# Optimization experiments

Measured on AMD Instinct MI355X. Metric: run time of the kernel, lower is better.

Reference implementation:

```python
import jax, jax.numpy as jnp
import numpy as np

EPS = 1e-5
SLOPE = 0.01  # torch LeakyReLU default negative_slope


def _stage(h, W):
    # h: [B, N, k, Cin]; W: [Cout, Cin] (1x1 conv, no bias)
    h = jnp.einsum('bnkc,oc->bnko', h, W)
    # InstanceNorm2d (affine=False): normalize per (batch, channel) over spatial (N, k)
    mean = jnp.mean(h, axis=(1, 2), keepdims=True)
    var = jnp.var(h, axis=(1, 2), keepdims=True)
    h = (h - mean) * jax.lax.rsqrt(var + EPS)
    return jnp.where(h >= 0, h, SLOPE * h)


def setup_inputs() -> dict:
    key = jax.random.key(0)
    k1, k2, k3, k4, k5 = jax.random.split(key, 5)
    B, N, D, K, C = 8, 4096, 64, 20, 64
    x = jax.random.normal(k1, (B, N, D), dtype=jnp.float32)
    ind = jax.random.randint(k2, (B, N, K), 0, B * N, dtype=jnp.int64)
    W1 = jax.random.normal(k3, (C, 2 * D), dtype=jnp.float32) * 0.05
    W2 = jax.random.normal(k4, (C, C), dtype=jnp.float32) * 0.05
    W3 = jax.random.normal(k5, (C, C), dtype=jnp.float32) * 0.05
    return {"x": x, "ind": ind, "W1": W1, "W2": W2, "W3": W3}


def reference(x, ind, W1, W2, W3):
    B, N, D = x.shape
    k = ind.shape[2]
    # Gather neighbors via global (B*N) indices, as in the torch code
    y = x.reshape(B * N, D)[ind.reshape(B * N, k)].reshape(B, N, k, D)  # [B,N,k,D]
    xe = jnp.broadcast_to(x[:, :, None, :], (B, N, k, D))
    feat = jnp.concatenate([y - xe, xe], axis=3)  # [B,N,k,2D]
    h = _stage(feat, W1)
    h = _stage(h, W2)
    h = _stage(h, W3)
    # max-pool over k neighbors -> [B, N, Cout]
    return jnp.max(h, axis=2)
```

## Files before the change

### kernel.cpp

```cpp
#include <hip/hip_runtime.h>

#define BDIM 8
#define NPTS 4096
#define KNEI 20
#define BN (BDIM*NPTS)
#define NKCNT (NPTS*KNEI)
#define EPSI 1e-5f
#define SLOPE 0.01f

typedef __attribute__((ext_vector_type(8))) short bf16x8;
typedef __attribute__((ext_vector_type(4))) float f32x4;
typedef __attribute__((ext_vector_type(4))) unsigned int u32x4;

__device__ __forceinline__ unsigned short f2bf(float f) {
    unsigned u = __builtin_bit_cast(unsigned, f);
    u += 0x7FFFu + ((u >> 16) & 1u);
    return (unsigned short)(u >> 16);
}
__device__ __forceinline__ float bf2f(unsigned short h) {
    unsigned u = ((unsigned)h) << 16;
    return __builtin_bit_cast(float, u);
}

__device__ __forceinline__ void async16(const void* g, void* l) {
    __builtin_amdgcn_global_load_lds(
        (const __attribute__((address_space(1))) unsigned int*)g,
        (__attribute__((address_space(3))) unsigned int*)l, 16, 0, 0);
}

__global__ __launch_bounds__(256) void k0_uv(const float* __restrict__ x,
        const float* __restrict__ W1, unsigned short* __restrict__ u,
        unsigned short* __restrict__ v) {
    __shared__ float wlds[64 * 129];
    __shared__ float xs[16 * 64];
    int tid = threadIdx.x;
    int m0 = blockIdx.x * 16;
    for (int i = tid; i < 8192; i += 256)
        wlds[(i >> 7) * 129 + (i & 127)] = W1[i];
    for (int i = tid; i < 1024; i += 256)
        xs[i] = x[m0 * 64 + i];
    __syncthreads();
    int o = tid & 63;
    int r0 = tid >> 6;
    float au[4] = {0.f, 0.f, 0.f, 0.f};
    float av[4] = {0.f, 0.f, 0.f, 0.f};
    for (int c = 0; c < 64; ++c) {
        float wa = wlds[o * 129 + c];
        float wb = wlds[o * 129 + 64 + c];
        float wd = wb - wa;
#pragma unroll
        for (int jj = 0; jj < 4; ++jj) {
            float xv = xs[(r0 + jj * 4) * 64 + c];
            au[jj] += xv * wa;
            av[jj] += xv * wd;
        }
    }
#pragma unroll
    for (int jj = 0; jj < 4; ++jj) {
        int m = m0 + r0 + jj * 4;
        u[m * 64 + o] = f2bf(au[jj]);
        v[m * 64 + o] = f2bf(av[jj]);
    }
}

__device__ __forceinline__ void load_bfrags(const float* __restrict__ W,
        int l15, int q, bf16x8 bw[4][2]) {
#pragma unroll
    for (int mt = 0; mt < 4; ++mt)
#pragma unroll
        for (int kc = 0; kc < 2; ++kc) {
            const float* wp = W + (mt * 16 + l15) * 64 + kc * 32 + q * 8;
            bf16x8 t;
#pragma unroll
            for (int j = 0; j < 8; ++j) t[j] = (short)f2bf(wp[j]);
            bw[mt][kc] = t;
        }
}

__global__ __launch_bounds__(256) void k1_stats1(const unsigned short* __restrict__ u,
        const unsigned short* __restrict__ v, const int* __restrict__ ind,
        float* __restrict__ s1) {
    __shared__ __align__(16) unsigned char tile[40960];
    __shared__ __align__(16) unsigned char vt[2048];
    __shared__ int inds[320];
    __shared__ float part[1024];
    int tid = threadIdx.x;
    int lane = tid & 63, w = tid >> 6;
    int b = blockIdx.x >> 8;
    int n0 = (blockIdx.x & 255) << 4;
    int base = b * NPTS + n0;
    int base20 = base * 20;
    for (int i = tid; i < 320; i += 256) inds[i] = ind[base20 + i];
    if (w == 0) {
#pragma unroll
        for (int k = 0; k < 2; ++k)
            async16(v + (size_t)(base + 8 * k + (lane >> 3)) * 64 + (lane & 7) * 8,
                    vt + k * 1024);
    }
    __syncthreads();
    int swz = (lane & 7) ^ ((lane >> 3) & 7);
#pragma unroll
    for (int j = 0; j < 10; ++j) {
        int k = w * 10 + j;
        int r = 8 * k + (lane >> 3);
        int idx = inds[r];
        async16(u + (size_t)idx * 64 + swz * 8, tile + k * 1024);
    }
    __syncthreads();
    int c2 = (tid & 31) * 2;
    int rr = tid >> 5;
    int uoff = (((c2 >> 3) ^ rr) << 4) + ((c2 * 2) & 15);
    float sA = 0.f, qA = 0.f, sB = 0.f, qB = 0.f;
    for (int j = 0; j < 40; ++j) {
        int r = rr + 8 * j;
        int p = (r * 3277) >> 16;
        unsigned uu = *(const unsigned*)(tile + r * 128 + uoff);
        unsigned vv = *(const unsigned*)(vt + p * 128 + c2 * 2);
        float h0 = bf2f((unsigned short)(uu & 0xFFFF)) + bf2f((unsigned short)(vv & 0xFFFF));
        float h1 = bf2f((unsigned short)(uu >> 16)) + bf2f((unsigned short)(vv >> 16));
        sA += h0; qA += h0 * h0;
        sB += h1; qB += h1 * h1;
    }
    part[tid * 4 + 0] = sA; part[tid * 4 + 1] = qA;
    part[tid * 4 + 2] = sB; part[tid * 4 + 3] = qB;
    __syncthreads();
    if (tid < 128) {
        int c = tid & 63, st = tid >> 6;
        float acc = 0.f;
        for (int g = 0; g < 8; ++g)
            acc += part[(g * 32 + (c >> 1)) * 4 + (c & 1) * 2 + st];
        atomicAdd(&s1[st * 512 + b * 64 + c], acc);
    }
}

__global__ __launch_bounds__(256) void k2_gemm2(const unsigned short* __restrict__ u,
        const unsigned short* __restrict__ v, const int* __restrict__ ind,
        const float* __restrict__ W2, const float* __restrict__ s1,
        float* __restrict__ s2, unsigned short* __restrict__ h2g) {
    __shared__ __align__(16) unsigned char tile[40960];
    __shared__ __align__(16) unsigned char vt[2048];
    __shared__ int inds[320];
    __shared__ float red[512];
    int tid = threadIdx.x;
    int lane = tid & 63, w = tid >> 6;
    int l15 = lane & 15, q = lane >> 4;
    int b = blockIdx.x >> 8;
    int n0 = (blockIdx.x & 255) << 4;
    int base = b * NPTS + n0;
    int base20 = base * 20;
    bf16x8 aw[4][2];
    load_bfrags(W2, l15, q, aw);
    const float inv = 1.0f / (float)NKCNT;
    float r1[2][8], mr1[2][8];
#pragma unroll
    for (int kc = 0; kc < 2; ++kc)
#pragma unroll
        for (int j = 0; j < 8; ++j) {
            int c = kc * 32 + q * 8 + j;
            float mm = s1[b * 64 + c] * inv;
            float vv = s1[512 + b * 64 + c] * inv - mm * mm;
            float rs = rsqrtf(vv + EPSI);
            r1[kc][j] = rs; mr1[kc][j] = -mm * rs;
        }
    for (int i = tid; i < 320; i += 256) inds[i] = ind[base20 + i];
    if (w == 0) {
#pragma unroll
        for (int k = 0; k < 2; ++k)
            async16(v + (size_t)(base + 8 * k + (lane >> 3)) * 64 + (lane & 7) * 8,
                    vt + k * 1024);
    }
    __syncthreads();
    int swz = (lane & 7) ^ ((lane >> 3) & 7);
#pragma unroll
    for (int j = 0; j < 10; ++j) {
        int k = w * 10 + j;
        int r = 8 * k + (lane >> 3);
        int idx = inds[r];
        async16(u + (size_t)idx * 64 + swz * 8, tile + k * 1024);
    }
    __syncthreads();
    bf16x8 bf[5][2];
#pragma unroll
    for (int nt = 0; nt < 5; ++nt) {
        int row = (w * 5 + nt) * 16 + l15;
        int p = (row * 3277) >> 16;
#pragma unroll
        for (int kc = 0; kc < 2; ++kc) {
            int phys = (((kc * 4 + q) ^ (row & 7)) << 4);
            bf16x8 ub = *(const bf16x8*)(tile + row * 128 + phys);
            bf16x8 vb = *(const bf16x8*)(vt + p * 128 + kc * 64 + q * 16);
            bf16x8 o;
#pragma unroll
            for (int j = 0; j < 8; ++j) {
                float hval = bf2f((unsigned short)ub[j]) + bf2f((unsigned short)vb[j]);
                float t = fmaf(hval, r1[kc][j], mr1[kc][j]);
                t = fmaxf(t, SLOPE * t);
                o[j] = (short)f2bf(t);
            }
            bf[nt][kc] = o;
        }
    }
    __syncthreads();
#pragma unroll
    for (int nt = 0; nt < 5; ++nt) {
        int row = (w * 5 + nt) * 16 + l15;
        int r7 = row & 7;
#pragma unroll
        for (int mt = 0; mt < 4; ++mt) {
            f32x4 acc = (f32x4){0.f, 0.f, 0.f, 0.f};
            acc = __builtin_amdgcn_mfma_f32_16x16x32_bf16(aw[mt][0], bf[nt][0], acc, 0, 0, 0);
            acc = __builtin_amdgcn_mfma_f32_16x16x32_bf16(aw[mt][1], bf[nt][1], acc, 0, 0, 0);
            unsigned long long pk =
                (unsigned long long)((unsigned)f2bf(acc[0]) | ((unsigned)f2bf(acc[1]) << 16)) |
                ((unsigned long long)((unsigned)f2bf(acc[2]) | ((unsigned)f2bf(acc[3]) << 16)) << 32);
            int chunk = mt * 2 + (q >> 1);
            int addr = row * 128 + (((chunk ^ r7)) << 4) + (q & 1) * 8;
            *(unsigned long long*)(tile + addr) = pk;
        }
    }
    __syncthreads();
    unsigned char* dstt = (unsigned char*)(h2g + (size_t)blockIdx.x * (320 * 64));
#pragma unroll
    for (int j2 = 0; j2 < 10; ++j2) {
        int off = j2 * 4096 + tid * 16;
        *(u32x4*)(dstt + off) = *(const u32x4*)(tile + off);
    }
    {
        int c = tid & 63, g = tid >> 6;
        int chunkc = c >> 3, inb = (c & 7) * 2;
        float ss = 0.f, qs = 0.f;
        for (int jj = 0; jj < 80; ++jj) {
            int row = g * 80 + jj;
            float f = bf2f(*(const unsigned short*)(tile + row * 128 +
                         ((chunkc ^ (row & 7)) << 4) + inb));
            ss += f; qs += f * f;
        }
        red[tid] = ss; red[256 + tid] = qs;
    }
    __syncthreads();
    if (tid < 64) {
        float a = 0.f, b2 = 0.f;
        for (int g2 = 0; g2 < 4; ++g2) {
            a  += red[g2 * 64 + tid];
            b2 += red[256 + g2 * 64 + tid];
        }
        atomicAdd(&s2[b * 64 + tid], a);
        atomicAdd(&s2[512 + b * 64 + tid], b2);
    }
}

__global__ __launch_bounds__(256) void k3_gemm3(const unsigned short* __restrict__ h2g,
        const float* __restrict__ W3, const float* __restrict__ s2,
        float* __restrict__ s3, float* __restrict__ out) {
    __shared__ __align__(16) unsigned char tile[40960];
    __shared__ float red[512];
    int tid = threadIdx.x;
    int lane = tid & 63, w = tid >> 6;
    int l15 = lane & 15, q = lane >> 4;
    int b = blockIdx.x >> 8;
    int n0 = (blockIdx.x & 255) << 4;
    int base = b * NPTS + n0;
    bf16x8 aw[4][2];
    load_bfrags(W3, l15, q, aw);
    const float inv = 1.0f / (float)NKCNT;
    float r2[2][8], mr2[2][8];
#pragma unroll
    for (int kc = 0; kc < 2; ++kc)
#pragma unroll
        for (int j = 0; j < 8; ++j) {
            int c = kc * 32 + q * 8 + j;
            float mm = s2[b * 64 + c] * inv;
            float vv = s2[512 + b * 64 + c] * inv - mm * mm;
            float rs = rsqrtf(vv + EPSI);
            r2[kc][j] = rs; mr2[kc][j] = -mm * rs;
        }
    const unsigned char* srct = (const unsigned char*)(h2g + (size_t)blockIdx.x * (320 * 64));
#pragma unroll
    for (int j = 0; j < 10; ++j) {
        int k = w * 10 + j;
        async16(srct + k * 1024 + lane * 16, tile + k * 1024);
    }
    __syncthreads();
    bf16x8 bf[5][2];
#pragma unroll
    for (int nt = 0; nt < 5; ++nt) {
        int row = (w * 5 + nt) * 16 + l15;
#pragma unroll
        for (int kc = 0; kc < 2; ++kc) {
            int phys = (((kc * 4 + q) ^ (row & 7)) << 4);
            bf16x8 hb = *(const bf16x8*)(tile + row * 128 + phys);
            bf16x8 o;
#pragma unroll
            for (int j = 0; j < 8; ++j) {
                float t = fmaf(bf2f((unsigned short)hb[j]), r2[kc][j], mr2[kc][j]);
                t = fmaxf(t, SLOPE * t);
                o[j] = (short)f2bf(t);
            }
            bf[nt][kc] = o;
        }
    }
    __syncthreads();
#pragma unroll
    for (int nt = 0; nt < 5; ++nt) {
        int row = (w * 5 + nt) * 16 + l15;
        int r7 = row & 7;
#pragma unroll
        for (int mt = 0; mt < 4; ++mt) {
            f32x4 acc = (f32x4){0.f, 0.f, 0.f, 0.f};
            acc = __builtin_amdgcn_mfma_f32_16x16x32_bf16(aw[mt][0], bf[nt][0], acc, 0, 0, 0);
            acc = __builtin_amdgcn_mfma_f32_16x16x32_bf16(aw[mt][1], bf[nt][1], acc, 0, 0, 0);
            unsigned long long pk =
                (unsigned long long)((unsigned)f2bf(acc[0]) | ((unsigned)f2bf(acc[1]) << 16)) |
                ((unsigned long long)((unsigned)f2bf(acc[2]) | ((unsigned)f2bf(acc[3]) << 16)) << 32);
            int chunk = mt * 2 + (q >> 1);
            int addr = row * 128 + (((chunk ^ r7)) << 4) + (q & 1) * 8;
            *(unsigned long long*)(tile + addr) = pk;
        }
    }
    __syncthreads();
    {
        int c = tid & 63, p0 = tid >> 6;
        int chunkc = c >> 3, inb = (c & 7) * 2;
        float ss = 0.f, qs = 0.f;
#pragma unroll
        for (int ii = 0; ii < 4; ++ii) {
            int p = p0 * 4 + ii;
            float mx = -3.4e38f;
            for (int kk = 0; kk < 20; ++kk) {
                int row = p * 20 + kk;
                float f = bf2f(*(const unsigned short*)(tile + row * 128 +
                             ((chunkc ^ (row & 7)) << 4) + inb));
                mx = fmaxf(mx, f);
                ss += f; qs += f * f;
            }
            out[(size_t)(base + p) * 64 + c] = mx;
        }
        red[tid] = ss; red[256 + tid] = qs;
    }
    __syncthreads();
    if (tid < 64) {
        float a = 0.f, b2 = 0.f;
        for (int g2 = 0; g2 < 4; ++g2) {
            a  += red[g2 * 64 + tid];
            b2 += red[256 + g2 * 64 + tid];
        }
        atomicAdd(&s3[b * 64 + tid], a);
        atomicAdd(&s3[512 + b * 64 + tid], b2);
    }
}

__global__ __launch_bounds__(256) void k4_final(float* __restrict__ out,
        const float* __restrict__ s3) {
    int idx = blockIdx.x * 256 + threadIdx.x;
    int c = idx & 63;
    int b = idx >> 18;
    const float inv = 1.0f / (float)NKCNT;
    float mm = s3[b * 64 + c] * inv;
    float vv = s3[512 + b * 64 + c] * inv - mm * mm;
    float r = rsqrtf(vv + EPSI);
    float val = (out[idx] - mm) * r;
    out[idx] = val >= 0.f ? val : SLOPE * val;
}

extern "C" void kernel_launch(void* const* d_in, const int* in_sizes, int n_in,
                              void* d_out, int out_size, void* d_ws, size_t ws_size,
                              hipStream_t stream) {
    const float* x   = (const float*)d_in[0];
    const int*   ind = (const int*)d_in[1];
    const float* W1  = (const float*)d_in[2];
    const float* W2  = (const float*)d_in[3];
    const float* W3  = (const float*)d_in[4];
    float* out = (float*)d_out;

    unsigned short* u = (unsigned short*)d_ws;
    unsigned short* v = u + BN * 64;
    float* stats = (float*)(v + BN * 64);
    float* s1 = stats;
    float* s2 = stats + 1024;
    float* s3 = stats + 2048;
    unsigned short* h2 = (unsigned short*)(stats + 3 * 1024);

    hipMemsetAsync(stats, 0, 3 * 1024 * sizeof(float), stream);
    k0_uv<<<dim3(BN / 16), dim3(256), 0, stream>>>(x, W1, u, v);
    k1_stats1<<<dim3(BN / 16), dim3(256), 0, stream>>>(u, v, ind, s1);
    k2_gemm2<<<dim3(BN / 16), dim3(256), 0, stream>>>(u, v, ind, W2, s1, s2, h2);
    k3_gemm3<<<dim3(BN / 16), dim3(256), 0, stream>>>(h2, W3, s2, s3, out);
    k4_final<<<dim3(BN * 64 / 256), dim3(256), 0, stream>>>(out, s3);
}
```

Measured before the change: 213.1 us.

## Recompute stage-2 GEMM instead of materializing h2 to global memory

```diff
diff --git a/kernel.cpp b/kernel.cpp
--- a/kernel.cpp
+++ b/kernel.cpp
@@ -133,10 +133,114 @@
     }
 }
 
-__global__ __launch_bounds__(256) void k2_gemm2(const unsigned short* __restrict__ u,
+__global__ __launch_bounds__(256) void k2_stats2(const unsigned short* __restrict__ u,
         const unsigned short* __restrict__ v, const int* __restrict__ ind,
         const float* __restrict__ W2, const float* __restrict__ s1,
-        float* __restrict__ s2, unsigned short* __restrict__ h2g) {
+        float* __restrict__ s2) {
+    __shared__ __align__(16) unsigned char tile[40960];
+    __shared__ __align__(16) unsigned char vt[2048];
+    __shared__ int inds[320];
+    int tid = threadIdx.x;
+    int lane = tid & 63, w = tid >> 6;
+    int l15 = lane & 15, q = lane >> 4;
+    int b = blockIdx.x >> 8;
+    int n0 = (blockIdx.x & 255) << 4;
+    int base = b * NPTS + n0;
+    int base20 = base * 20;
+    bf16x8 aw[4][2];
+    load_bfrags(W2, l15, q, aw);
+    const float inv = 1.0f / (float)NKCNT;
+    float r1[2][8], mr1[2][8];
+#pragma unroll
+    for (int kc = 0; kc < 2; ++kc)
+#pragma unroll
+        for (int j = 0; j < 8; ++j) {
+            int c = kc * 32 + q * 8 + j;
+            float mm = s1[b * 64 + c] * inv;
+            float vv = s1[512 + b * 64 + c] * inv - mm * mm;
+            float rs = rsqrtf(vv + EPSI);
+            r1[kc][j] = rs; mr1[kc][j] = -mm * rs;
+        }
+    for (int i = tid; i < 320; i += 256) inds[i] = ind[base20 + i];
+    if (w == 0) {
+#pragma unroll
+        for (int k = 0; k < 2; ++k)
+            async16(v + (size_t)(base + 8 * k + (lane >> 3)) * 64 + (lane & 7) * 8,
+                    vt + k * 1024);
+    }
+    __syncthreads();
+    int swz = (lane & 7) ^ ((lane >> 3) & 7);
+#pragma unroll
+    for (int j = 0; j < 10; ++j) {
+        int k = w * 10 + j;
+        int r = 8 * k + (lane >> 3);
+        int idx = inds[r];
+        async16(u + (size_t)idx * 64 + swz * 8, tile + k * 1024);
+    }
+    __syncthreads();
+    bf16x8 bf[5][2];
+#pragma unroll
+    for (int nt = 0; nt < 5; ++nt) {
+        int row = (w * 5 + nt) * 16 + l15;
+        int p = (row * 3277) >> 16;
+#pragma unroll
+        for (int kc = 0; kc < 2; ++kc) {
+            int phys = (((kc * 4 + q) ^ (row & 7)) << 4);
+            bf16x8 ub = *(const bf16x8*)(tile + row * 128 + phys);
+            bf16x8 vb = *(const bf16x8*)(vt + p * 128 + kc * 64 + q * 16);
+            bf16x8 o;
+#pragma unroll
+            for (int j = 0; j < 8; ++j) {
+                float hval = bf2f((unsigned short)ub[j]) + bf2f((unsigned short)vb[j]);
+                float t = fmaf(hval, r1[kc][j], mr1[kc][j]);
+                t = fmaxf(t, SLOPE * t);
+                o[j] = (short)f2bf(t);
+            }
+            bf[nt][kc] = o;
+        }
+    }
+    float ss[16], qq[16];
+#pragma unroll
+    for (int e = 0; e < 16; ++e) { ss[e] = 0.f; qq[e] = 0.f; }
+#pragma unroll
+    for (int nt = 0; nt < 5; ++nt) {
+#pragma unroll
+        for (int mt = 0; mt < 4; ++mt) {
+            f32x4 acc = (f32x4){0.f, 0.f, 0.f, 0.f};
+            acc = __builtin_amdgcn_mfma_f32_16x16x32_bf16(aw[mt][0], bf[nt][0], acc, 0, 0, 0);
+            acc = __builtin_amdgcn_mfma_f32_16x16x32_bf16(aw[mt][1], bf[nt][1], acc, 0, 0, 0);
+#pragma unroll
+            for (int i = 0; i < 4; ++i) {
+                ss[mt * 4 + i] += acc[i];
+                qq[mt * 4 + i] = fmaf(acc[i], acc[i], qq[mt * 4 + i]);
+            }
+        }
+    }
+    __syncthreads();
+    float* ssp = (float*)tile;
+    float* qqp = ssp + 64 * 68;
+#pragma unroll
+    for (int e = 0; e < 16; ++e) {
+        int cout = (e >> 2) * 16 + q * 4 + (e & 3);
+        int idx = cout * 68 + w * 16 + l15;
+        ssp[idx] = ss[e]; qqp[idx] = qq[e];
+    }
+    __syncthreads();
+    if (tid < 128) {
+        int st = tid >> 6, c = tid & 63;
+        const float* arr = st ? qqp : ssp;
+        float a = 0.f;
+        for (int j = 0; j < 64; ++j)
+            a += arr[c * 68 + ((j + c) & 63)];
+        atomicAdd(&s2[st * 512 + b * 64 + c], a);
+    }
+}
+
+__global__ __launch_bounds__(256) void k3_gemm3(const unsigned short* __restrict__ u,
+        const unsigned short* __restrict__ v, const int* __restrict__ ind,
+        const float* __restrict__ W2, const float* __restrict__ W3,
+        const float* __restrict__ s1, const float* __restrict__ s2,
+        float* __restrict__ s3, float* __restrict__ out) {
     __shared__ __align__(16) unsigned char tile[40960];
     __shared__ __align__(16) unsigned char vt[2048];
     __shared__ int inds[320];
@@ -162,6 +266,15 @@
             float rs = rsqrtf(vv + EPSI);
             r1[kc][j] = rs; mr1[kc][j] = -mm * rs;
         }
+    float r2c[16], mr2c[16];
+#pragma unroll
+    for (int e = 0; e < 16; ++e) {
+        int c = (e >> 2) * 16 + q * 4 + (e & 3);
+        float mm = s2[b * 64 + c] * inv;
+        float vv = s2[512 + b * 64 + c] * inv - mm * mm;
+        float rs = rsqrtf(vv + EPSI);
+        r2c[e] = rs; mr2c[e] = -mm * rs;
+    }
     for (int i = tid; i < 320; i += 256) inds[i] = ind[base20 + i];
     if (w == 0) {
 #pragma unroll
@@ -210,110 +323,40 @@
             f32x4 acc = (f32x4){0.f, 0.f, 0.f, 0.f};
             acc = __builtin_amdgcn_mfma_f32_16x16x32_bf16(aw[mt][0], bf[nt][0], acc, 0, 0, 0);
             acc = __builtin_amdgcn_mfma_f32_16x16x32_bf16(aw[mt][1], bf[nt][1], acc, 0, 0, 0);
+            unsigned short e0, e1, e2, e3;
+            {
+                float t0 = fmaf(acc[0], r2c[mt * 4 + 0], mr2c[mt * 4 + 0]); t0 = fmaxf(t0, SLOPE * t0);
+                float t1 = fmaf(acc[1], r2c[mt * 4 + 1], mr2c[mt * 4 + 1]); t1 = fmaxf(t1, SLOPE * t1);
+                float t2 = fmaf(acc[2], r2c[mt * 4 + 2], mr2c[mt * 4 + 2]); t2 = fmaxf(t2, SLOPE * t2);
+                float t3 = fmaf(acc[3], r2c[mt * 4 + 3], mr2c[mt * 4 + 3]); t3 = fmaxf(t3, SLOPE * t3);
+                e0 = f2bf(t0); e1 = f2bf(t1); e2 = f2bf(t2); e3 = f2bf(t3);
+            }
+            unsigned long long pk =
+                (unsigned long long)((unsigned)e0 | ((unsigned)e1 << 16)) |
+                ((unsigned long long)((unsigned)e2 | ((unsigned)e3 << 16)) << 32);
+            int chunk = mt * 2 + (q >> 1);
+            int addr = row * 128 + ((chunk ^ r7) << 4) + (q & 1) * 8;
+            *(unsigned long long*)(tile + addr) = pk;
+        }
+    }
+    load_bfrags(W3, l15, q, aw);
+    __syncthreads();
+#pragma unroll
+    for (int nt = 0; nt < 5; ++nt) {
+        int row = (w * 5 + nt) * 16 + l15;
+        int r7 = row & 7;
+        bf16x8 b0 = *(const bf16x8*)(tile + row * 128 + (((0 + q) ^ r7) << 4));
+        bf16x8 b1 = *(const bf16x8*)(tile + row * 128 + (((4 + q) ^ r7) << 4));
+#pragma unroll
+        for (int mt = 0; mt < 4; ++mt) {
+            f32x4 acc = (f32x4){0.f, 0.f, 0.f, 0.f};
+            acc = __builtin_amdgcn_mfma_f32_16x16x32_bf16(aw[mt][0], b0, acc, 0, 0, 0);
+            acc = __builtin_amdgcn_mfma_f32_16x16x32_bf16(aw[mt][1], b1, acc, 0, 0, 0);
             unsigned long long pk =
                 (unsigned long long)((unsigned)f2bf(acc[0]) | ((unsigned)f2bf(acc[1]) << 16)) |
                 ((unsigned long long)((unsigned)f2bf(acc[2]) | ((unsigned)f2bf(acc[3]) << 16)) << 32);
             int chunk = mt * 2 + (q >> 1);
-            int addr = row * 128 + (((chunk ^ r7)) << 4) + (q & 1) * 8;
-            *(unsigned long long*)(tile + addr) = pk;
-        }
-    }
-    __syncthreads();
-    unsigned char* dstt = (unsigned char*)(h2g + (size_t)blockIdx.x * (320 * 64));
-#pragma unroll
-    for (int j2 = 0; j2 < 10; ++j2) {
-        int off = j2 * 4096 + tid * 16;
-        *(u32x4*)(dstt + off) = *(const u32x4*)(tile + off);
-    }
-    {
-        int c = tid & 63, g = tid >> 6;
-        int chunkc = c >> 3, inb = (c & 7) * 2;
-        float ss = 0.f, qs = 0.f;
-        for (int jj = 0; jj < 80; ++jj) {
-            int row = g * 80 + jj;
-            float f = bf2f(*(const unsigned short*)(tile + row * 128 +
-                         ((chunkc ^ (row & 7)) << 4) + inb));
-            ss += f; qs += f * f;
-        }
-        red[tid] = ss; red[256 + tid] = qs;
-    }
-    __syncthreads();
-    if (tid < 64) {
-        float a = 0.f, b2 = 0.f;
-        for (int g2 = 0; g2 < 4; ++g2) {
-            a  += red[g2 * 64 + tid];
-            b2 += red[256 + g2 * 64 + tid];
-        }
-        atomicAdd(&s2[b * 64 + tid], a);
-        atomicAdd(&s2[512 + b * 64 + tid], b2);
-    }
-}
-
-__global__ __launch_bounds__(256) void k3_gemm3(const unsigned short* __restrict__ h2g,
-        const float* __restrict__ W3, const float* __restrict__ s2,
-        float* __restrict__ s3, float* __restrict__ out) {
-    __shared__ __align__(16) unsigned char tile[40960];
-    __shared__ float red[512];
-    int tid = threadIdx.x;
-    int lane = tid & 63, w = tid >> 6;
-    int l15 = lane & 15, q = lane >> 4;
-    int b = blockIdx.x >> 8;
-    int n0 = (blockIdx.x & 255) << 4;
-    int base = b * NPTS + n0;
-    bf16x8 aw[4][2];
-    load_bfrags(W3, l15, q, aw);
-    const float inv = 1.0f / (float)NKCNT;
-    float r2[2][8], mr2[2][8];
-#pragma unroll
-    for (int kc = 0; kc < 2; ++kc)
-#pragma unroll
-        for (int j = 0; j < 8; ++j) {
-            int c = kc * 32 + q * 8 + j;
-            float mm = s2[b * 64 + c] * inv;
-            float vv = s2[512 + b * 64 + c] * inv - mm * mm;
-            float rs = rsqrtf(vv + EPSI);
-            r2[kc][j] = rs; mr2[kc][j] = -mm * rs;
-        }
-    const unsigned char* srct = (const unsigned char*)(h2g + (size_t)blockIdx.x * (320 * 64));
-#pragma unroll
-    for (int j = 0; j < 10; ++j) {
-        int k = w * 10 + j;
-        async16(srct + k * 1024 + lane * 16, tile + k * 1024);
-    }
-    __syncthreads();
-    bf16x8 bf[5][2];
-#pragma unroll
-    for (int nt = 0; nt < 5; ++nt) {
-        int row = (w * 5 + nt) * 16 + l15;
-#pragma unroll
-        for (int kc = 0; kc < 2; ++kc) {
-            int phys = (((kc * 4 + q) ^ (row & 7)) << 4);
-            bf16x8 hb = *(const bf16x8*)(tile + row * 128 + phys);
-            bf16x8 o;
-#pragma unroll
-            for (int j = 0; j < 8; ++j) {
-                float t = fmaf(bf2f((unsigned short)hb[j]), r2[kc][j], mr2[kc][j]);
-                t = fmaxf(t, SLOPE * t);
-                o[j] = (short)f2bf(t);
-            }
-            bf[nt][kc] = o;
-        }
-    }
-    __syncthreads();
-#pragma unroll
-    for (int nt = 0; nt < 5; ++nt) {
-        int row = (w * 5 + nt) * 16 + l15;
-        int r7 = row & 7;
-#pragma unroll
-        for (int mt = 0; mt < 4; ++mt) {
-            f32x4 acc = (f32x4){0.f, 0.f, 0.f, 0.f};
-            acc = __builtin_amdgcn_mfma_f32_16x16x32_bf16(aw[mt][0], bf[nt][0], acc, 0, 0, 0);
-            acc = __builtin_amdgcn_mfma_f32_16x16x32_bf16(aw[mt][1], bf[nt][1], acc, 0, 0, 0);
-            unsigned long long pk =
-                (unsigned long long)((unsigned)f2bf(acc[0]) | ((unsigned)f2bf(acc[1]) << 16)) |
-                ((unsigned long long)((unsigned)f2bf(acc[2]) | ((unsigned)f2bf(acc[3]) << 16)) << 32);
-            int chunk = mt * 2 + (q >> 1);
-            int addr = row * 128 + (((chunk ^ r7)) << 4) + (q & 1) * 8;
+            int addr = row * 128 + ((chunk ^ r7) << 4) + (q & 1) * 8;
             *(unsigned long long*)(tile + addr) = pk;
         }
     }
@@ -321,7 +364,7 @@
     {
         int c = tid & 63, p0 = tid >> 6;
         int chunkc = c >> 3, inb = (c & 7) * 2;
-        float ss = 0.f, qs = 0.f;
+        float ssv = 0.f, qsv = 0.f;
 #pragma unroll
         for (int ii = 0; ii < 4; ++ii) {
             int p = p0 * 4 + ii;
@@ -331,11 +374,11 @@
                 float f = bf2f(*(const unsigned short*)(tile + row * 128 +
                              ((chunkc ^ (row & 7)) << 4) + inb));
                 mx = fmaxf(mx, f);
-                ss += f; qs += f * f;
+                ssv += f; qsv += f * f;
             }
             out[(size_t)(base + p) * 64 + c] = mx;
         }
-        red[tid] = ss; red[256 + tid] = qs;
+        red[tid] = ssv; red[256 + tid] = qsv;
     }
     __syncthreads();
     if (tid < 64) {
@@ -378,12 +421,11 @@
     float* s1 = stats;
     float* s2 = stats + 1024;
     float* s3 = stats + 2048;
-    unsigned short* h2 = (unsigned short*)(stats + 3 * 1024);
 
     hipMemsetAsync(stats, 0, 3 * 1024 * sizeof(float), stream);
     k0_uv<<<dim3(BN / 16), dim3(256), 0, stream>>>(x, W1, u, v);
     k1_stats1<<<dim3(BN / 16), dim3(256), 0, stream>>>(u, v, ind, s1);
-    k2_gemm2<<<dim3(BN / 16), dim3(256), 0, stream>>>(u, v, ind, W2, s1, s2, h2);
-    k3_gemm3<<<dim3(BN / 16), dim3(256), 0, stream>>>(h2, W3, s2, s3, out);
+    k2_stats2<<<dim3(BN / 16), dim3(256), 0, stream>>>(u, v, ind, W2, s1, s2);
+    k3_gemm3<<<dim3(BN / 16), dim3(256), 0, stream>>>(u, v, ind, W2, W3, s1, s2, s3, out);
     k4_final<<<dim3(BN * 64 / 256), dim3(256), 0, stream>>>(out, s3);
 }
```

After: 241.8 us. 13.5% more time.
